# Kernel tuning notes

Measured on AMD Instinct MI355X. Metric: run time of the kernel, lower is better.

The kernel has to match this reference:

```python
import jax, jax.numpy as jnp
import numpy as np

L, B, D = 2048, 4, 1024
H = 16
DK = D // 2            # q/k dim = 512
GLU_D = 2816
D_CONV = 4
NORMALIZER = 16.0
EPS = 1e-5


def setup_inputs() -> dict:
    key = jax.random.key(0)
    ks = jax.random.split(key, 20)
    s = 0.02
    inp = {
        "x": jax.random.normal(ks[0], (L, B, D), jnp.float32),
        "tn_w": jnp.ones((D,), jnp.float32),
        "tn_b": jnp.zeros((D,), jnp.float32),
        "conv_w": jax.random.normal(ks[1], (D, D_CONV), jnp.float32) * s,  # depthwise kernel (d, w)
        "q_w": jax.random.normal(ks[2], (D, DK), jnp.float32) * s,
        "kg_w": jax.random.normal(ks[3], (D, DK), jnp.float32) * s,
        "v_w": jax.random.normal(ks[4], (D, D), jnp.float32) * s,
        "g_w": jax.random.normal(ks[5], (D, D), jnp.float32) * s,
        "g_b": jnp.zeros((D,), jnp.float32),
        "out_w": jax.random.normal(ks[6], (D, D), jnp.float32) * s,
        "aug_balance": jax.random.normal(ks[7], (DK,), jnp.float32) * s,
        "cn_w": jnp.ones((D,), jnp.float32),
        "cn_b": jnp.zeros((D,), jnp.float32),
        "l1_w": jax.random.normal(ks[8], (D, GLU_D), jnp.float32) * s,
        "l2_w": jax.random.normal(ks[9], (D, GLU_D), jnp.float32) * s,
        "l3_w": jax.random.normal(ks[10], (GLU_D, D), jnp.float32) * s,
    }
    return inp


def _layernorm(y, w, b):
    m = jnp.mean(y, axis=-1, keepdims=True)
    v = jnp.var(y, axis=-1, keepdims=True)
    return (y - m) * jax.lax.rsqrt(v + EPS) * w + b


def _gla_scan(q, k, v, gk):
    # q,k,gk: (B,H,L,dk); v: (B,H,L,dv). Recurrent gated linear attention:
    # S_t = diag(exp(gk_t)) S_{t-1} + k_t v_t^T ; o_t = q_t S_t
    b, h, l, dk = q.shape
    dv = v.shape[-1]
    qT = jnp.moveaxis(q, 2, 0)  # (L,B,H,dk)
    kT = jnp.moveaxis(k, 2, 0)
    vT = jnp.moveaxis(v, 2, 0)
    gT = jnp.moveaxis(gk, 2, 0)

    def step(S, inp):
        q_t, k_t, v_t, g_t = inp
        S = jnp.exp(g_t)[..., None] * S + k_t[..., :, None] * v_t[..., None, :]
        o_t = jnp.einsum('bhk,bhkv->bhv', q_t, S)
        return S, o_t

    S0 = jnp.zeros((b, h, dk, dv), jnp.float32)
    _, o = jax.lax.scan(step, S0, (qT, kT, vT, gT))  # o: (L,B,H,dv)
    return jnp.moveaxis(o, 0, 2)  # (B,H,L,dv)


def reference(x, tn_w, tn_b, conv_w, q_w, kg_w, v_w, g_w, g_b, out_w,
              aug_balance, cn_w, cn_b, l1_w, l2_w, l3_w):
    residual = x  # (L,B,D)
    h = _layernorm(x, tn_w, tn_b)
    h = jnp.transpose(h, (1, 0, 2))  # (B,L,D)

    # causal depthwise conv1d (kernel 4, left pad 3) + SiLU
    hp = jnp.pad(h, ((0, 0), (D_CONV - 1, 0), (0, 0)))
    y = sum(hp[:, i:i + L, :] * conv_w[:, i] for i in range(D_CONV))
    y = jax.nn.silu(y)

    q = y @ q_w                     # (B,L,DK)
    kg = y @ kg_w                   # (B,L,DK)
    v = y @ v_w                     # (B,L,D)
    g = y @ g_w + g_b               # (B,L,D)

    gk = jax.nn.log_sigmoid(kg) / NORMALIZER
    k = 1.0 - jnp.exp(gk)

    dk_h = DK // H   # 32
    dv_h = D // H    # 64
    qh = q.reshape(B, L, H, dk_h).transpose(0, 2, 1, 3).astype(jnp.float32)
    kh = k.reshape(B, L, H, dk_h).transpose(0, 2, 1, 3).astype(jnp.float32)
    vh = v.reshape(B, L, H, dv_h).transpose(0, 2, 1, 3).astype(jnp.float32)
    gh = gk.reshape(B, L, H, dk_h).transpose(0, 2, 1, 3).astype(jnp.float32)
    aug = aug_balance.reshape(H, dk_h).astype(jnp.float32)

    o = _gla_scan(qh, kh, vh, gh)  # (B,H,L,dv_h)

    # self-augmentation term
    aug_w = jnp.einsum('bhld,hd,bhld->bhl', qh, aug, kh)
    o = o + jax.nn.sigmoid(aug_w[..., None] * vh)

    # group norm: LayerNorm over head dim, no affine
    m = jnp.mean(o, axis=-1, keepdims=True)
    var = jnp.var(o, axis=-1, keepdims=True)
    o = (o - m) * jax.lax.rsqrt(var + EPS)
    o = o.transpose(0, 2, 1, 3).reshape(B, L, D).astype(x.dtype)

    o = jax.nn.silu(g) * o
    o = o @ out_w                   # (B,L,D)

    x1 = jnp.transpose(o, (1, 0, 2)) + residual  # back to (L,B,D)

    z = _layernorm(x1, cn_w, cn_b)
    glu = (jax.nn.silu(z @ l1_w) * (z @ l2_w)) @ l3_w
    return glu + x1
```

## Files before the change

kernel.cpp:

```cpp
#include <hip/hip_runtime.h>


#define Lseq 2048
#define Bb 4
#define Dd 1024
#define Hh 16
#define GLUD 2816
#define NC 32
#define CHK 64

typedef float f32x4 __attribute__((ext_vector_type(4)));
typedef __bf16 bf16x8 __attribute__((ext_vector_type(8)));
typedef unsigned short u16;
typedef u16 u16x8 __attribute__((ext_vector_type(8)));

__device__ __forceinline__ u16 f2bf(float f) {
  unsigned int u = __float_as_uint(f);
  u += 0x7fffu + ((u >> 16) & 1u);
  return (u16)(u >> 16);
}

__device__ __forceinline__ void gll16(const void* g, void* l) {
  __builtin_amdgcn_global_load_lds((const __attribute__((address_space(1))) void*)g,
                                   (__attribute__((address_space(3))) void*)l, 16, 0, 0);
}

__device__ __forceinline__ float block_sum(float v, float* red) {
#pragma unroll
  for (int o = 32; o > 0; o >>= 1) v += __shfl_down(v, o);
  __syncthreads();
  if ((threadIdx.x & 63) == 0) red[threadIdx.x >> 6] = v;
  __syncthreads();
  return red[0] + red[1] + red[2] + red[3];
}

__global__ __launch_bounds__(256) void ln1_k(const float* __restrict__ x,
                                             const float* __restrict__ w,
                                             const float* __restrict__ bia,
                                             float* __restrict__ h) {
  __shared__ float red[4];
  int r = blockIdx.x;
  int l = r >> 2, bb = r & 3;
  const float* xr = x + (size_t)r * Dd;
  int d0 = threadIdx.x * 4;
  float4 xv = *(const float4*)&xr[d0];
  float mean = block_sum(xv.x + xv.y + xv.z + xv.w, red) * (1.f / Dd);
  float a0 = xv.x - mean, a1 = xv.y - mean, a2 = xv.z - mean, a3 = xv.w - mean;
  float var = block_sum(a0 * a0 + a1 * a1 + a2 * a2 + a3 * a3, red) * (1.f / Dd);
  float rs = rsqrtf(var + 1e-5f);
  float4 ov;
  ov.x = a0 * rs * w[d0 + 0] + bia[d0 + 0];
  ov.y = a1 * rs * w[d0 + 1] + bia[d0 + 1];
  ov.z = a2 * rs * w[d0 + 2] + bia[d0 + 2];
  ov.w = a3 * rs * w[d0 + 3] + bia[d0 + 3];
  *(float4*)&h[((size_t)(bb * Lseq + l)) * Dd + d0] = ov;
}

__global__ __launch_bounds__(256) void ln2_k(const float* __restrict__ x1,
                                             const float* __restrict__ w,
                                             const float* __restrict__ bia,
                                             u16* __restrict__ z) {
  __shared__ float red[4];
  int r = blockIdx.x;
  const float* xr = x1 + (size_t)r * Dd;
  int d0 = threadIdx.x * 4;
  float4 xv = *(const float4*)&xr[d0];
  float mean = block_sum(xv.x + xv.y + xv.z + xv.w, red) * (1.f / Dd);
  float a0 = xv.x - mean, a1 = xv.y - mean, a2 = xv.z - mean, a3 = xv.w - mean;
  float var = block_sum(a0 * a0 + a1 * a1 + a2 * a2 + a3 * a3, red) * (1.f / Dd);
  float rs = rsqrtf(var + 1e-5f);
  ushort4 o;
  o.x = f2bf(a0 * rs * w[d0 + 0] + bia[d0 + 0]);
  o.y = f2bf(a1 * rs * w[d0 + 1] + bia[d0 + 1]);
  o.z = f2bf(a2 * rs * w[d0 + 2] + bia[d0 + 2]);
  o.w = f2bf(a3 * rs * w[d0 + 3] + bia[d0 + 3]);
  *(ushort4*)&z[(size_t)r * Dd + d0] = o;
}

__global__ __launch_bounds__(256) void conv_k(const float* __restrict__ h,
                                              const float* __restrict__ cw,
                                              u16* __restrict__ ybf) {
  int m = blockIdx.x;
  int b = m >> 11, l = m & (Lseq - 1);
  int d0 = threadIdx.x * 4;
  float4 acc = {0.f, 0.f, 0.f, 0.f};
  const float* hb = h + ((size_t)b * Lseq) * Dd + d0;
#pragma unroll
  for (int w = 0; w < 4; w++) {
    int ll = l - 3 + w;
    if (ll >= 0) {
      float4 hv = *(const float4*)&hb[(size_t)ll * Dd];
      acc.x += hv.x * cw[(d0 + 0) * 4 + w];
      acc.y += hv.y * cw[(d0 + 1) * 4 + w];
      acc.z += hv.z * cw[(d0 + 2) * 4 + w];
      acc.w += hv.w * cw[(d0 + 3) * 4 + w];
    }
  }
  ushort4 o;
  o.x = f2bf(acc.x / (1.f + expf(-acc.x)));
  o.y = f2bf(acc.y / (1.f + expf(-acc.y)));
  o.z = f2bf(acc.z / (1.f + expf(-acc.z)));
  o.w = f2bf(acc.w / (1.f + expf(-acc.w)));
  *(ushort4*)&ybf[(size_t)m * Dd + d0] = o;
}

__global__ __launch_bounds__(256) void transpose_bf16(const float* __restrict__ src,
                                                      u16* __restrict__ dst,
                                                      int R, int C, int mult, int off) {
  __shared__ float tile[32][33];
  int tx = threadIdx.x & 31, ty = threadIdx.x >> 5;
  int c0 = blockIdx.x * 32, r0 = blockIdx.y * 32;
#pragma unroll
  for (int k = 0; k < 4; k++)
    tile[ty + 8 * k][tx] = src[(size_t)(r0 + ty + 8 * k) * C + c0 + tx];
  __syncthreads();
#pragma unroll
  for (int k = 0; k < 4; k++) {
    int c = c0 + ty + 8 * k;
    dst[(size_t)(c * mult + off) * R + r0 + tx] = f2bf(tile[tx][ty + 8 * k]);
  }
}

__global__ __launch_bounds__(256) void gate_k(const float* __restrict__ qkvg,
                                              float* __restrict__ decay) {
  int idx = blockIdx.x * 256 + threadIdx.x;
  int m = idx >> 9, d = idx & 511;
  float kg = qkvg[(size_t)m * 3072 + 512 + d];
  float s = 1.f / (1.f + expf(-kg));
  decay[idx] = expf(0.0625f * logf(s));
}

__global__ __launch_bounds__(256) void passA_k(const float* __restrict__ decay,
                                               const float* __restrict__ qkvg,
                                               float* __restrict__ T,
                                               float* __restrict__ P) {
  int wave = threadIdx.x >> 6, lane = threadIdx.x & 63;
  int c = blockIdx.x * 4 + wave, bh = blockIdx.y;
  int b = bh >> 4, h = bh & 15;
  size_t t0 = (size_t)b * Lseq + c * CHK;
  const float* ep = decay + t0 * 512 + h * 32;
  const float* vp = qkvg + t0 * 3072 + 1024 + h * 64 + lane;
  const float* dp = decay + t0 * 512 + h * 32 + (lane & 31);
  float S[32];
#pragma unroll
  for (int i = 0; i < 32; i++) S[i] = 0.f;
  float p = 1.f;
  float vnext = vp[0], dnext = dp[0];
#pragma unroll 1
  for (int ts = 0; ts < CHK; ts++) {
    float vj = vnext, dl = dnext;
    int tn = (ts + 1 < CHK) ? ts + 1 : ts;
    vnext = vp[(size_t)tn * 3072];
    dnext = dp[(size_t)tn * 512];
    const float* e = ep + (size_t)ts * 512;
    p *= dl;
#pragma unroll
    for (int i = 0; i < 32; i++) {
      float ei = e[i];
      float kv = (1.f - ei) * vj;
      S[i] = ei * S[i] + kv;
    }
  }
  float* Tc = T + ((size_t)bh * NC + c) * 2048;
#pragma unroll
  for (int i = 0; i < 32; i++) Tc[i * 64 + lane] = S[i];
  if (lane < 32) P[((size_t)bh * NC + c) * 32 + lane] = p;
}

__global__ __launch_bounds__(256) void passB_k(const float* __restrict__ T,
                                               const float* __restrict__ P,
                                               float* __restrict__ Sg) {
  int bh = blockIdx.x;
  int tid = threadIdx.x;
  int f = tid * 8, i = f >> 6;
  float s[8];
#pragma unroll
  for (int e = 0; e < 8; e++) s[e] = 0.f;
  for (int c = 0; c < NC; c++) {
    size_t base = ((size_t)bh * NC + c) * 2048 + f;
    float pc = P[((size_t)bh * NC + c) * 32 + i];
#pragma unroll
    for (int e = 0; e < 8; e++) {
      Sg[base + e] = s[e];
      s[e] = pc * s[e] + T[base + e];
    }
  }
}

__global__ __launch_bounds__(256) void passC_k(const float* __restrict__ decay,
                                               const float* __restrict__ qkvg,
                                               const float* __restrict__ Sg,
                                               float* __restrict__ osc) {
  int wave = threadIdx.x >> 6, lane = threadIdx.x & 63;
  int c = blockIdx.x * 4 + wave, bh = blockIdx.y;
  int b = bh >> 4, h = bh & 15;
  size_t t0 = (size_t)b * Lseq + c * CHK;
  const float* ep = decay + t0 * 512 + h * 32;
  const float* qp = qkvg + t0 * 3072 + h * 32;
  const float* vp = qkvg + t0 * 3072 + 1024 + h * 64 + lane;
  float* op = osc + t0 * 1024 + h * 64 + lane;
  float S[32];
  const float* Sgc = Sg + ((size_t)bh * NC + c) * 2048;
#pragma unroll
  for (int i = 0; i < 32; i++) S[i] = Sgc[i * 64 + lane];
  float vnext = vp[0];
#pragma unroll 1
  for (int ts = 0; ts < CHK; ts++) {
    float vj = vnext;
    int tn = (ts + 1 < CHK) ? ts + 1 : ts;
    vnext = vp[(size_t)tn * 3072];
    const float* e = ep + (size_t)ts * 512;
    const float* q = qp + (size_t)ts * 3072;
    float a0 = 0.f, a1 = 0.f, a2 = 0.f, a3 = 0.f;
#pragma unroll
    for (int i = 0; i < 32; i += 4) {
      float e0 = e[i], e1 = e[i + 1], e2 = e[i + 2], e3 = e[i + 3];
      S[i + 0] = e0 * S[i + 0] + (1.f - e0) * vj; a0 += q[i + 0] * S[i + 0];
      S[i + 1] = e1 * S[i + 1] + (1.f - e1) * vj; a1 += q[i + 1] * S[i + 1];
      S[i + 2] = e2 * S[i + 2] + (1.f - e2) * vj; a2 += q[i + 2] * S[i + 2];
      S[i + 3] = e3 * S[i + 3] + (1.f - e3) * vj; a3 += q[i + 3] * S[i + 3];
    }
    op[(size_t)ts * 1024] = (a0 + a1) + (a2 + a3);
  }
}

__global__ __launch_bounds__(256) void postscan_k(const float* __restrict__ osc,
                                                  const float* __restrict__ qkvg,
                                                  const float* __restrict__ decay,
                                                  const float* __restrict__ aug,
                                                  const float* __restrict__ gb,
                                                  u16* __restrict__ o2) {
  int m = blockIdx.x;
  int tid = threadIdx.x;
  int h = tid >> 4, t16 = tid & 15;
  int j0 = t16 * 4;
  size_t base = (size_t)m * 3072;
  float4 ov = *(const float4*)&osc[(size_t)m * 1024 + h * 64 + j0];
  int i0 = t16 * 2;
  float q0 = qkvg[base + h * 32 + i0], q1 = qkvg[base + h * 32 + i0 + 1];
  float kA = 1.f - decay[(size_t)m * 512 + h * 32 + i0];
  float kB = 1.f - decay[(size_t)m * 512 + h * 32 + i0 + 1];
  float aw = q0 * aug[h * 32 + i0] * kA + q1 * aug[h * 32 + i0 + 1] * kB;
  aw += __shfl_xor(aw, 1); aw += __shfl_xor(aw, 2);
  aw += __shfl_xor(aw, 4); aw += __shfl_xor(aw, 8);
  float4 vv = *(const float4*)&qkvg[base + 1024 + h * 64 + j0];
  ov.x += 1.f / (1.f + expf(-aw * vv.x));
  ov.y += 1.f / (1.f + expf(-aw * vv.y));
  ov.z += 1.f / (1.f + expf(-aw * vv.z));
  ov.w += 1.f / (1.f + expf(-aw * vv.w));
  float s = ov.x + ov.y + ov.z + ov.w;
  s += __shfl_xor(s, 1); s += __shfl_xor(s, 2);
  s += __shfl_xor(s, 4); s += __shfl_xor(s, 8);
  float mean = s * (1.f / 64.f);
  float d0 = ov.x - mean, d1 = ov.y - mean, d2 = ov.z - mean, d3 = ov.w - mean;
  float ss = d0 * d0 + d1 * d1 + d2 * d2 + d3 * d3;
  ss += __shfl_xor(ss, 1); ss += __shfl_xor(ss, 2);
  ss += __shfl_xor(ss, 4); ss += __shfl_xor(ss, 8);
  float rs = rsqrtf(ss * (1.f / 64.f) + 1e-5f);
  float4 gv = *(const float4*)&qkvg[base + 2048 + h * 64 + j0];
  float g0 = gv.x + gb[h * 64 + j0 + 0];
  float g1 = gv.y + gb[h * 64 + j0 + 1];
  float g2 = gv.z + gb[h * 64 + j0 + 2];
  float g3 = gv.w + gb[h * 64 + j0 + 3];
  ushort4 o;
  o.x = f2bf((g0 / (1.f + expf(-g0))) * d0 * rs);
  o.y = f2bf((g1 / (1.f + expf(-g1))) * d1 * rs);
  o.z = f2bf((g2 / (1.f + expf(-g2))) * d2 * rs);
  o.w = f2bf((g3 / (1.f + expf(-g3))) * d3 * rs);
  *(ushort4*)&o2[(size_t)m * 1024 + h * 64 + j0] = o;
}

template <int EPI>
__global__ __launch_bounds__(256) void gemm_bt(const u16* __restrict__ A,
                                               const u16* __restrict__ B,
                                               int M, int N, int K,
                                               float* __restrict__ Cf,
                                               const float* __restrict__ addsrc,
                                               u16* __restrict__ Cbf) {
  __shared__ __align__(16) u16 lA[128 * 32];
  __shared__ __align__(16) u16 lB[128 * 32];
  const int tid = threadIdx.x;
  const int wave = tid >> 6, lane = tid & 63;
  const int m0 = blockIdx.y * 128, n0 = blockIdx.x * 128;
  const int wm = wave & 1, wn = wave >> 1;
  f32x4 acc[4][4];
#pragma unroll
  for (int a = 0; a < 4; a++)
#pragma unroll
    for (int b = 0; b < 4; b++) acc[a][b] = {0.f, 0.f, 0.f, 0.f};

  const int srow = lane >> 2;
  const int sk8 = (lane & 3) * 8;
  const int kofs = (lane >> 4) * 8;
  const int rsel = lane & 15;
  for (int k0 = 0; k0 < K; k0 += 32) {
    __syncthreads();
#pragma unroll
    for (int it = 0; it < 2; it++) {
      int j = wave * 2 + it;
      int row = j * 16 + srow;
      gll16(A + (size_t)(m0 + row) * K + k0 + sk8, &lA[j * 512]);
      gll16(B + (size_t)(n0 + row) * K + k0 + sk8, &lB[j * 512]);
    }
    __syncthreads();
    bf16x8 af[4], bfr[4];
#pragma unroll
    for (int t = 0; t < 4; t++) {
      af[t] = __builtin_bit_cast(bf16x8, *(const u16x8*)&lA[(wm * 64 + t * 16 + rsel) * 32 + kofs]);
      bfr[t] = __builtin_bit_cast(bf16x8, *(const u16x8*)&lB[(wn * 64 + t * 16 + rsel) * 32 + kofs]);
    }
#pragma unroll
    for (int tm = 0; tm < 4; tm++)
#pragma unroll
      for (int tn = 0; tn < 4; tn++)
        acc[tm][tn] = __builtin_amdgcn_mfma_f32_16x16x32_bf16(af[tm], bfr[tn], acc[tm][tn], 0, 0, 0);
  }

  const int rquad = (lane >> 4) * 4;
  const int csel = lane & 15;
#pragma unroll
  for (int tm = 0; tm < 4; tm++) {
    int rowb = m0 + wm * 64 + tm * 16 + rquad;
#pragma unroll
    for (int tn = 0; tn < 4; tn++) {
      int col = n0 + wn * 64 + tn * 16 + csel;
#pragma unroll
      for (int r = 0; r < 4; r++) {
        float v = acc[tm][tn][r];
        int row = rowb + r;
        if (EPI == 0) {
          Cf[(size_t)row * N + col] = v;
        } else if (EPI == 1) {
          int l = row & (Lseq - 1), bb = row >> 11;
          size_t o = ((size_t)(l * Bb + bb)) * Dd + col;
          Cf[o] = v + addsrc[o];
        } else if (EPI == 2) {
          size_t o = (size_t)row * Dd + col;
          Cf[o] = v + addsrc[o];
        } else {
          float partner = __shfl_xor(v, 1);
          if ((lane & 1) == 0) {
            float p = (v / (1.f + expf(-v))) * partner;
            Cbf[(size_t)row * (N >> 1) + (col >> 1)] = f2bf(p);
          }
        }
      }
    }
  }
}

extern "C" void kernel_launch(void* const* d_in, const int* in_sizes, int n_in,
                              void* d_out, int out_size, void* d_ws, size_t ws_size,
                              hipStream_t stream) {
  const float* x = (const float*)d_in[0];
  const float* tn_w = (const float*)d_in[1];
  const float* tn_b = (const float*)d_in[2];
  const float* conv_w = (const float*)d_in[3];
  const float* q_w = (const float*)d_in[4];
  const float* kg_w = (const float*)d_in[5];
  const float* v_w = (const float*)d_in[6];
  const float* g_w = (const float*)d_in[7];
  const float* g_b = (const float*)d_in[8];
  const float* out_w = (const float*)d_in[9];
  const float* aug = (const float*)d_in[10];
  const float* cn_w = (const float*)d_in[11];
  const float* cn_b = (const float*)d_in[12];
  const float* l1_w = (const float*)d_in[13];
  const float* l2_w = (const float*)d_in[14];
  const float* l3_w = (const float*)d_in[15];
  float* out = (float*)d_out;
  char* ws = (char*)d_ws;

  u16* Wqkvg = (u16*)(ws + 0);
  u16* Wout = (u16*)(ws + 6291456);
  u16* Wl12 = (u16*)(ws + 8388608);
  u16* Wl3 = (u16*)(ws + 19922944);
  float* hbuf = (float*)(ws + 25690112);
  float* osc = hbuf;
  u16* ybf = (u16*)(ws + 59244544);
  float* Sg = (float*)(ws + 59244544);
  u16* o2bf = (u16*)(ws + 59244544);
  float* qkvg = (float*)(ws + 76021760);
  float* x1 = (float*)(ws + 76021760);
  u16* zbf = (u16*)(ws + 109576192);
  u16* pbf = (u16*)(ws + 126353408);
  float* decay = (float*)(ws + 176685056);
  float* Tbuf = (float*)(ws + 193462272);
  float* Pbuf = (float*)(ws + 210239488);

  dim3 b256(256);
  transpose_bf16<<<dim3(16, 32), b256, 0, stream>>>(q_w, Wqkvg, 1024, 512, 1, 0);
  transpose_bf16<<<dim3(16, 32), b256, 0, stream>>>(kg_w, Wqkvg + 512 * 1024, 1024, 512, 1, 0);
  transpose_bf16<<<dim3(32, 32), b256, 0, stream>>>(v_w, Wqkvg + 1024 * 1024, 1024, 1024, 1, 0);
  transpose_bf16<<<dim3(32, 32), b256, 0, stream>>>(g_w, Wqkvg + 2048 * 1024, 1024, 1024, 1, 0);
  transpose_bf16<<<dim3(32, 32), b256, 0, stream>>>(out_w, Wout, 1024, 1024, 1, 0);
  transpose_bf16<<<dim3(88, 32), b256, 0, stream>>>(l1_w, Wl12, 1024, 2816, 2, 0);
  transpose_bf16<<<dim3(88, 32), b256, 0, stream>>>(l2_w, Wl12, 1024, 2816, 2, 1);
  transpose_bf16<<<dim3(32, 88), b256, 0, stream>>>(l3_w, Wl3, 2816, 1024, 1, 0);

  ln1_k<<<8192, b256, 0, stream>>>(x, tn_w, tn_b, hbuf);
  conv_k<<<8192, b256, 0, stream>>>(hbuf, conv_w, ybf);
  gemm_bt<0><<<dim3(24, 64), b256, 0, stream>>>(ybf, Wqkvg, 8192, 3072, 1024, qkvg, nullptr, nullptr);
  gate_k<<<16384, b256, 0, stream>>>(qkvg, decay);
  passA_k<<<dim3(NC / 4, 64), b256, 0, stream>>>(decay, qkvg, Tbuf, Pbuf);
  passB_k<<<64, b256, 0, stream>>>(Tbuf, Pbuf, Sg);
  passC_k<<<dim3(NC / 4, 64), b256, 0, stream>>>(decay, qkvg, Sg, osc);
  postscan_k<<<8192, b256, 0, stream>>>(osc, qkvg, decay, aug, g_b, o2bf);
  gemm_bt<1><<<dim3(8, 64), b256, 0, stream>>>(o2bf, Wout, 8192, 1024, 1024, x1, x, nullptr);
  ln2_k<<<8192, b256, 0, stream>>>(x1, cn_w, cn_b, zbf);
  gemm_bt<3><<<dim3(44, 64), b256, 0, stream>>>(zbf, Wl12, 8192, 5632, 1024, nullptr, nullptr, pbf);
  gemm_bt<2><<<dim3(8, 64), b256, 0, stream>>>(pbf, Wl3, 8192, 1024, 2816, out, x1, nullptr);
}
```

Before: 755.6 us.

## Swizzle bf16 GEMM operands, fuse gate into GEMM epilogue, merge weight transposes

Producers of the bf16 GEMM operands now write with an XOR-style column rotation, so the MFMA fragment loads from LDS read rotated offsets and avoid bank conflicts. The decay gate computation moves into the QKVG GEMM epilogue, which removes the separate gate kernel and the round trip through the kg columns. The eight weight transpose launches become one combined prep kernel. The GLU epilogue pairs tiles within a thread instead of using lane shuffles, and Sg now aliases the T buffer. Every producer and consumer has to agree on the swizzle, which adds risk.

```diff
diff --git a/kernel.cpp b/kernel.cpp
--- a/kernel.cpp
+++ b/kernel.cpp
@@ -18,6 +18,10 @@
   unsigned int u = __float_as_uint(f);
   u += 0x7fffu + ((u >> 16) & 1u);
   return (u16)(u >> 16);
+}
+
+__device__ __forceinline__ int swz(int col, int row) {
+  return (col & ~31) | ((((col >> 3) + (row >> 1)) & 3) << 3) | (col & 7);
 }
 
 __device__ __forceinline__ void gll16(const void* g, void* l) {
@@ -74,7 +78,8 @@
   o.y = f2bf(a1 * rs * w[d0 + 1] + bia[d0 + 1]);
   o.z = f2bf(a2 * rs * w[d0 + 2] + bia[d0 + 2]);
   o.w = f2bf(a3 * rs * w[d0 + 3] + bia[d0 + 3]);
-  *(ushort4*)&z[(size_t)r * Dd + d0] = o;
+  int dcol = (d0 & ~31) | ((((d0 >> 3) + (r >> 1)) & 3) << 3) | (d0 & 7);
+  *(ushort4*)&z[(size_t)r * Dd + dcol] = o;
 }
 
 __global__ __launch_bounds__(256) void conv_k(const float* __restrict__ h,
@@ -101,15 +106,40 @@
   o.y = f2bf(acc.y / (1.f + expf(-acc.y)));
   o.z = f2bf(acc.z / (1.f + expf(-acc.z)));
   o.w = f2bf(acc.w / (1.f + expf(-acc.w)));
-  *(ushort4*)&ybf[(size_t)m * Dd + d0] = o;
-}
-
-__global__ __launch_bounds__(256) void transpose_bf16(const float* __restrict__ src,
-                                                      u16* __restrict__ dst,
-                                                      int R, int C, int mult, int off) {
+  int dcol = (d0 & ~31) | ((((d0 >> 3) + (m >> 1)) & 3) << 3) | (d0 & 7);
+  *(ushort4*)&ybf[(size_t)m * Dd + dcol] = o;
+}
+
+__global__ __launch_bounds__(256) void prep_k(const float* __restrict__ q_w,
+                                              const float* __restrict__ kg_w,
+                                              const float* __restrict__ v_w,
+                                              const float* __restrict__ g_w,
+                                              const float* __restrict__ out_w,
+                                              const float* __restrict__ l1_w,
+                                              const float* __restrict__ l2_w,
+                                              const float* __restrict__ l3_w,
+                                              u16* __restrict__ Wqkvg,
+                                              u16* __restrict__ Wout,
+                                              u16* __restrict__ Wl12,
+                                              u16* __restrict__ Wl3) {
   __shared__ float tile[32][33];
+  int blk = blockIdx.x;
+  const float* src;
+  u16* dst;
+  int R, C, ilv = 0, off = 0, base;
+  if (blk < 512)       { src = q_w;   dst = Wqkvg;              R = 1024; C = 512;  base = 0; }
+  else if (blk < 1024) { src = kg_w;  dst = Wqkvg + 512 * 1024; R = 1024; C = 512;  base = 512; }
+  else if (blk < 2048) { src = v_w;   dst = Wqkvg + 1024 * 1024; R = 1024; C = 1024; base = 1024; }
+  else if (blk < 3072) { src = g_w;   dst = Wqkvg + 2048 * 1024; R = 1024; C = 1024; base = 2048; }
+  else if (blk < 4096) { src = out_w; dst = Wout;               R = 1024; C = 1024; base = 3072; }
+  else if (blk < 6912) { src = l1_w;  dst = Wl12; R = 1024; C = 2816; ilv = 1; off = 0; base = 4096; }
+  else if (blk < 9728) { src = l2_w;  dst = Wl12; R = 1024; C = 2816; ilv = 1; off = 1; base = 6912; }
+  else                 { src = l3_w;  dst = Wl3;  R = 2816; C = 1024; base = 9728; }
+  int local = blk - base;
+  int ct = C >> 5;
+  int bx = local % ct, by = local / ct;
   int tx = threadIdx.x & 31, ty = threadIdx.x >> 5;
-  int c0 = blockIdx.x * 32, r0 = blockIdx.y * 32;
+  int c0 = bx * 32, r0 = by * 32;
 #pragma unroll
   for (int k = 0; k < 4; k++)
     tile[ty + 8 * k][tx] = src[(size_t)(r0 + ty + 8 * k) * C + c0 + tx];
@@ -117,17 +147,10 @@
 #pragma unroll
   for (int k = 0; k < 4; k++) {
     int c = c0 + ty + 8 * k;
-    dst[(size_t)(c * mult + off) * R + r0 + tx] = f2bf(tile[tx][ty + 8 * k]);
-  }
-}
-
-__global__ __launch_bounds__(256) void gate_k(const float* __restrict__ qkvg,
-                                              float* __restrict__ decay) {
-  int idx = blockIdx.x * 256 + threadIdx.x;
-  int m = idx >> 9, d = idx & 511;
-  float kg = qkvg[(size_t)m * 3072 + 512 + d];
-  float s = 1.f / (1.f + expf(-kg));
-  decay[idx] = expf(0.0625f * logf(s));
+    int dstrow = ilv ? (((c >> 4) << 5) + off * 16 + (c & 15)) : c;
+    int kpos = r0 + tx;
+    dst[(size_t)dstrow * R + swz(kpos, dstrow)] = f2bf(tile[tx][ty + 8 * k]);
+  }
 }
 
 __global__ __launch_bounds__(256) void passA_k(const float* __restrict__ decay,
@@ -181,8 +204,9 @@
     float pc = P[((size_t)bh * NC + c) * 32 + i];
 #pragma unroll
     for (int e = 0; e < 8; e++) {
+      float tv = T[base + e];
       Sg[base + e] = s[e];
-      s[e] = pc * s[e] + T[base + e];
+      s[e] = pc * s[e] + tv;
     }
   }
 }
@@ -267,7 +291,9 @@
   o.y = f2bf((g1 / (1.f + expf(-g1))) * d1 * rs);
   o.z = f2bf((g2 / (1.f + expf(-g2))) * d2 * rs);
   o.w = f2bf((g3 / (1.f + expf(-g3))) * d3 * rs);
-  *(ushort4*)&o2[(size_t)m * 1024 + h * 64 + j0] = o;
+  int col = h * 64 + j0;
+  int dcol = (col & ~31) | ((((col >> 3) + (m >> 1)) & 3) << 3) | (col & 7);
+  *(ushort4*)&o2[(size_t)m * 1024 + dcol] = o;
 }
 
 template <int EPI>
@@ -276,7 +302,8 @@
                                                int M, int N, int K,
                                                float* __restrict__ Cf,
                                                const float* __restrict__ addsrc,
-                                               u16* __restrict__ Cbf) {
+                                               u16* __restrict__ Cbf,
+                                               float* __restrict__ decayp) {
   __shared__ __align__(16) u16 lA[128 * 32];
   __shared__ __align__(16) u16 lB[128 * 32];
   const int tid = threadIdx.x;
@@ -291,8 +318,8 @@
 
   const int srow = lane >> 2;
   const int sk8 = (lane & 3) * 8;
-  const int kofs = (lane >> 4) * 8;
   const int rsel = lane & 15;
+  const int rot = (((lane >> 4) + (rsel >> 1)) & 3) << 3;
   for (int k0 = 0; k0 < K; k0 += 32) {
     __syncthreads();
 #pragma unroll
@@ -306,8 +333,8 @@
     bf16x8 af[4], bfr[4];
 #pragma unroll
     for (int t = 0; t < 4; t++) {
-      af[t] = __builtin_bit_cast(bf16x8, *(const u16x8*)&lA[(wm * 64 + t * 16 + rsel) * 32 + kofs]);
-      bfr[t] = __builtin_bit_cast(bf16x8, *(const u16x8*)&lB[(wn * 64 + t * 16 + rsel) * 32 + kofs]);
+      af[t] = __builtin_bit_cast(bf16x8, *(const u16x8*)&lA[(wm * 64 + t * 16 + rsel) * 32 + rot]);
+      bfr[t] = __builtin_bit_cast(bf16x8, *(const u16x8*)&lB[(wn * 64 + t * 16 + rsel) * 32 + rot]);
     }
 #pragma unroll
     for (int tm = 0; tm < 4; tm++)
@@ -329,7 +356,12 @@
         float v = acc[tm][tn][r];
         int row = rowb + r;
         if (EPI == 0) {
-          Cf[(size_t)row * N + col] = v;
+          if (col >= 512 && col < 1024) {
+            float sg = 1.f / (1.f + expf(-v));
+            decayp[(size_t)row * 512 + (col - 512)] = expf(0.0625f * logf(sg));
+          } else {
+            Cf[(size_t)row * N + col] = v;
+          }
         } else if (EPI == 1) {
           int l = row & (Lseq - 1), bb = row >> 11;
           size_t o = ((size_t)(l * Bb + bb)) * Dd + col;
@@ -338,10 +370,11 @@
           size_t o = (size_t)row * Dd + col;
           Cf[o] = v + addsrc[o];
         } else {
-          float partner = __shfl_xor(v, 1);
-          if ((lane & 1) == 0) {
-            float p = (v / (1.f + expf(-v))) * partner;
-            Cbf[(size_t)row * (N >> 1) + (col >> 1)] = f2bf(p);
+          if ((tn & 1) == 0) {
+            float u2 = acc[tm][tn + 1][r];
+            float p = (v / (1.f + expf(-v))) * u2;
+            int oc = (n0 >> 1) + wn * 32 + ((tn >> 1) << 4) + csel;
+            Cbf[(size_t)row * (N >> 1) + swz(oc, row)] = f2bf(p);
           }
         }
       }
@@ -378,7 +411,6 @@
   float* hbuf = (float*)(ws + 25690112);
   float* osc = hbuf;
   u16* ybf = (u16*)(ws + 59244544);
-  float* Sg = (float*)(ws + 59244544);
   u16* o2bf = (u16*)(ws + 59244544);
   float* qkvg = (float*)(ws + 76021760);
   float* x1 = (float*)(ws + 76021760);
@@ -386,28 +418,21 @@
   u16* pbf = (u16*)(ws + 126353408);
   float* decay = (float*)(ws + 176685056);
   float* Tbuf = (float*)(ws + 193462272);
+  float* Sg = Tbuf;
   float* Pbuf = (float*)(ws + 210239488);
 
   dim3 b256(256);
-  transpose_bf16<<<dim3(16, 32), b256, 0, stream>>>(q_w, Wqkvg, 1024, 512, 1, 0);
-  transpose_bf16<<<dim3(16, 32), b256, 0, stream>>>(kg_w, Wqkvg + 512 * 1024, 1024, 512, 1, 0);
-  transpose_bf16<<<dim3(32, 32), b256, 0, stream>>>(v_w, Wqkvg + 1024 * 1024, 1024, 1024, 1, 0);
-  transpose_bf16<<<dim3(32, 32), b256, 0, stream>>>(g_w, Wqkvg + 2048 * 1024, 1024, 1024, 1, 0);
-  transpose_bf16<<<dim3(32, 32), b256, 0, stream>>>(out_w, Wout, 1024, 1024, 1, 0);
-  transpose_bf16<<<dim3(88, 32), b256, 0, stream>>>(l1_w, Wl12, 1024, 2816, 2, 0);
-  transpose_bf16<<<dim3(88, 32), b256, 0, stream>>>(l2_w, Wl12, 1024, 2816, 2, 1);
-  transpose_bf16<<<dim3(32, 88), b256, 0, stream>>>(l3_w, Wl3, 2816, 1024, 1, 0);
-
+  prep_k<<<12544, b256, 0, stream>>>(q_w, kg_w, v_w, g_w, out_w, l1_w, l2_w, l3_w,
+                                     Wqkvg, Wout, Wl12, Wl3);
   ln1_k<<<8192, b256, 0, stream>>>(x, tn_w, tn_b, hbuf);
   conv_k<<<8192, b256, 0, stream>>>(hbuf, conv_w, ybf);
-  gemm_bt<0><<<dim3(24, 64), b256, 0, stream>>>(ybf, Wqkvg, 8192, 3072, 1024, qkvg, nullptr, nullptr);
-  gate_k<<<16384, b256, 0, stream>>>(qkvg, decay);
+  gemm_bt<0><<<dim3(24, 64), b256, 0, stream>>>(ybf, Wqkvg, 8192, 3072, 1024, qkvg, nullptr, nullptr, decay);
   passA_k<<<dim3(NC / 4, 64), b256, 0, stream>>>(decay, qkvg, Tbuf, Pbuf);
   passB_k<<<64, b256, 0, stream>>>(Tbuf, Pbuf, Sg);
   passC_k<<<dim3(NC / 4, 64), b256, 0, stream>>>(decay, qkvg, Sg, osc);
   postscan_k<<<8192, b256, 0, stream>>>(osc, qkvg, decay, aug, g_b, o2bf);
-  gemm_bt<1><<<dim3(8, 64), b256, 0, stream>>>(o2bf, Wout, 8192, 1024, 1024, x1, x, nullptr);
+  gemm_bt<1><<<dim3(8, 64), b256, 0, stream>>>(o2bf, Wout, 8192, 1024, 1024, x1, x, nullptr, nullptr);
   ln2_k<<<8192, b256, 0, stream>>>(x1, cn_w, cn_b, zbf);
-  gemm_bt<3><<<dim3(44, 64), b256, 0, stream>>>(zbf, Wl12, 8192, 5632, 1024, nullptr, nullptr, pbf);
-  gemm_bt<2><<<dim3(8, 64), b256, 0, stream>>>(pbf, Wl3, 8192, 1024, 2816, out, x1, nullptr);
-}
+  gemm_bt<3><<<dim3(44, 64), b256, 0, stream>>>(zbf, Wl12, 8192, 5632, 1024, nullptr, nullptr, pbf, nullptr);
+  gemm_bt<2><<<dim3(8, 64), b256, 0, stream>>>(pbf, Wl3, 8192, 1024, 2816, out, x1, nullptr, nullptr);
+}
```

New measurement: 732.0 us. 1.03x faster.
